# Kernel optimization log

Measured on AMD Instinct MI355X. Metric: run time of the kernel, lower is better.

Reference implementation:

```python
import jax, jax.numpy as jnp
import numpy as np

N, D = 8192, 128


def setup_inputs() -> dict:
    key = jax.random.key(0)
    k1, k2 = jax.random.split(key)
    z1 = jax.random.normal(k1, (N, D), dtype=jnp.float32)
    z2 = jax.random.normal(k2, (N, D), dtype=jnp.float32)
    return {"z1": z1, "z2": z2}


def reference(z1, z2):
    # logits[i, j] = -||z1_i - z2_j||^2, computed via the cdist-as-GEMM identity
    # (same math as dz = z2[None,:,:] - z1[:,None,:]; -einsum('...d,...d->...', dz, dz))
    sq1 = jnp.sum(z1 * z1, axis=-1)  # [N]
    sq2 = jnp.sum(z2 * z2, axis=-1)  # [N]
    logits = 2.0 * (z1 @ z2.T) - sq1[:, None] - sq2[None, :]  # [N, N]
    # CrossEntropyLoss with labels = arange(N): mean over rows of -log_softmax diag
    logp = jax.nn.log_softmax(logits, axis=-1)
    return -jnp.mean(jnp.diagonal(logp))
```

## Files before the change

kernel.cpp:

```cpp
#include <hip/hip_runtime.h>
#include <hip/hip_bf16.h>

typedef unsigned int   u32;
typedef unsigned short u16;

#define NN   8192
#define DD   128
#define CCH  32
#define CHUNK (NN / CCH)
#define JT   64
#define NT   (CHUNK / JT)
#define NIB  (NN / 256)

#define LOG2E 1.4426950408889634f
#define LN2F  0.6931471805599453f
#define BIAS  32.0f

typedef __bf16 bf16x8 __attribute__((ext_vector_type(8)));
typedef float  f32x16 __attribute__((ext_vector_type(16)));
typedef float  f32x2  __attribute__((ext_vector_type(2)));

__device__ __forceinline__ u16 f2bf(float x) {
    u32 u = __float_as_uint(x);
    u += 0x7fffu + ((u >> 16) & 1u);
    return (u16)(u >> 16);
}

__global__ __launch_bounds__(256) void prep_kernel(
    const float* __restrict__ z1, const float* __restrict__ z2,
    u32* __restrict__ b1, u32* __restrict__ b2,
    float* __restrict__ negsq2b, float* __restrict__ diag, u32* __restrict__ ctrl)
{
    if (blockIdx.x == 0 && threadIdx.x == 0) ctrl[0] = 0;
    int row  = blockIdx.x * 4 + (threadIdx.x >> 6);
    int lane = threadIdx.x & 63;
    float2 a = reinterpret_cast<const float2*>(z1)[row * 64 + lane];
    float2 b = reinterpret_cast<const float2*>(z2)[row * 64 + lane];
    b1[row * 64 + lane] = (u32)f2bf(a.x) | ((u32)f2bf(a.y) << 16);
    b2[row * 64 + lane] = (u32)f2bf(b.x) | ((u32)f2bf(b.y) << 16);
    float dot = a.x * b.x + a.y * b.y;
    float sq  = b.x * b.x + b.y * b.y;
    #pragma unroll
    for (int o = 32; o > 0; o >>= 1) {
        dot += __shfl_xor(dot, o);
        sq  += __shfl_xor(sq, o);
    }
    if (lane == 0) {
        negsq2b[row] = -sq * LOG2E - BIAS;
        diag[row]    = 2.0f * dot - sq;
    }
}

__global__ __launch_bounds__(256) void score_kernel(
    const u16* __restrict__ b1, const u16* __restrict__ b2,
    const float* __restrict__ negsq2b, float* __restrict__ partS)
{
    __shared__ alignas(16) u16 tile[3][JT * DD];
    __shared__ alignas(16) float nqs[CHUNK];
    const int tid  = threadIdx.x;
    const int lane = tid & 63;
    const int wid  = tid >> 6;
    const int r    = lane & 31, hi = lane >> 5;

    const int f     = blockIdx.x;
    const int chunk = (f >> 3) & 31;
    const int iblk  = (f & 7) * 4 + (f >> 8);
    const int j0    = chunk * CHUNK;
    const int i0w   = iblk * 256 + wid * 64;

    bf16x8 zf0[8], zf1[8];
    #pragma unroll
    for (int kk = 0; kk < 8; ++kk) {
        zf0[kk] = *reinterpret_cast<const bf16x8*>(b1 + (size_t)(i0w + r)      * DD + kk * 16 + hi * 8);
        zf1[kk] = *reinterpret_cast<const bf16x8*>(b1 + (size_t)(i0w + 32 + r) * DD + kk * 16 + hi * 8);
    }
    nqs[tid] = negsq2b[j0 + tid];
    __syncthreads();

    const int sl   = lane & 15;
    const int rrow = lane >> 4;

    auto stage = [&](int t, u16* dst_base) {
        #pragma unroll
        for (int u = 0; u < 4; ++u) {
            int row   = wid * 16 + u * 4 + rrow;
            int gslot = sl ^ (row & 15);
            const u16* src = b2 + (size_t)(j0 + t * JT + row) * DD + gslot * 8;
            __builtin_amdgcn_global_load_lds(
                (const __attribute__((address_space(1))) void*)src,
                (__attribute__((address_space(3))) void*)(dst_base + (wid * 16 + u * 4) * DD),
                16, 0, 0);
        }
    };

    stage(0, tile[0]);
    stage(1, tile[1]);

    float s0 = 0.f, s1 = 0.f, s2 = 0.f, s3 = 0.f;
    const f32x2 C2v = {2.0f * LOG2E, 2.0f * LOG2E};
    const int sw = r & 15;

    #pragma unroll
    for (int t = 0; t < NT; ++t) {
        if (t < NT - 1) asm volatile("s_waitcnt vmcnt(4)" ::: "memory");
        else            asm volatile("s_waitcnt vmcnt(0)" ::: "memory");
        __builtin_amdgcn_s_barrier();
        __builtin_amdgcn_sched_barrier(0);
        if (t + 2 < NT) stage(t + 2, tile[(t + 2) % 3]);
        const u16* tp = tile[t % 3];
        #pragma unroll
        for (int jj = 0; jj < 2; ++jj) {
            const float* nqb = &nqs[t * JT + jj * 32 + 4 * hi];
            float4 nq0 = *reinterpret_cast<const float4*>(nqb);
            float4 nq1 = *reinterpret_cast<const float4*>(nqb + 8);
            float4 nq2 = *reinterpret_cast<const float4*>(nqb + 16);
            float4 nq3 = *reinterpret_cast<const float4*>(nqb + 24);
            bf16x8 av[8];
            #pragma unroll
            for (int kk = 0; kk < 8; ++kk) {
                int off = (jj * 32 + r) * DD + (((2 * kk + hi) ^ sw) << 3);
                av[kk] = *reinterpret_cast<const bf16x8*>(tp + off);
            }
            f32x16 acc0 = {0.f}; f32x16 acc1 = {0.f};
            __builtin_amdgcn_s_setprio(1);
            #pragma unroll
            for (int kk = 0; kk < 8; ++kk) {
                acc0 = __builtin_amdgcn_mfma_f32_32x32x16_bf16(av[kk], zf0[kk], acc0, 0, 0, 0);
                acc1 = __builtin_amdgcn_mfma_f32_32x32x16_bf16(av[kk], zf1[kk], acc1, 0, 0, 0);
            }
            __builtin_amdgcn_s_setprio(0);
            const float nqa[16] = {nq0.x, nq0.y, nq0.z, nq0.w,
                                   nq1.x, nq1.y, nq1.z, nq1.w,
                                   nq2.x, nq2.y, nq2.z, nq2.w,
                                   nq3.x, nq3.y, nq3.z, nq3.w};
            #pragma unroll
            for (int q = 0; q < 8; ++q) {
                f32x2 n2 = {nqa[2 * q], nqa[2 * q + 1]};
                f32x2 a0 = {acc0[2 * q], acc0[2 * q + 1]};
                f32x2 t0 = a0 * C2v + n2;
                s0 += __builtin_amdgcn_exp2f(t0.x);
                s1 += __builtin_amdgcn_exp2f(t0.y);
                f32x2 a1 = {acc1[2 * q], acc1[2 * q + 1]};
                f32x2 t1 = a1 * C2v + n2;
                s2 += __builtin_amdgcn_exp2f(t1.x);
                s3 += __builtin_amdgcn_exp2f(t1.y);
            }
        }
    }

    float sum0 = s0 + s1, sum1 = s2 + s3;
    sum0 += __shfl_xor(sum0, 32);
    sum1 += __shfl_xor(sum1, 32);
    if (hi == 0) {
        partS[(size_t)chunk * NN + i0w + r]      = sum0;
        partS[(size_t)chunk * NN + i0w + 32 + r] = sum1;
    }
}

__global__ __launch_bounds__(256) void finalize1_kernel(
    const float* __restrict__ partS, const float* __restrict__ diag,
    float* __restrict__ blocksum, u32* __restrict__ ctrl, float* __restrict__ out)
{
    __shared__ float red[4];
    __shared__ u32 ticket;
    int r = blockIdx.x * 256 + threadIdx.x;
    float s = 0.f;
    #pragma unroll
    for (int c = 0; c < CCH; ++c) s += partS[(size_t)c * NN + r];
    float lse = (BIAS + __builtin_amdgcn_logf(s)) * LN2F;
    float acc = lse - diag[r];
    #pragma unroll
    for (int o = 32; o > 0; o >>= 1) acc += __shfl_xor(acc, o);
    int lane = threadIdx.x & 63, wid = threadIdx.x >> 6;
    if (lane == 0) red[wid] = acc;
    __syncthreads();
    if (threadIdx.x == 0) {
        blocksum[blockIdx.x] = red[0] + red[1] + red[2] + red[3];
        __threadfence();
        ticket = atomicAdd(ctrl, 1u);
    }
    __syncthreads();
    if (ticket == NIB - 1 && threadIdx.x == 0) {
        __threadfence();
        float v = 0.f;
        #pragma unroll
        for (int c = 0; c < NIB; ++c) v += blocksum[c];
        out[0] = v * (1.0f / (float)NN);
    }
}

extern "C" void kernel_launch(void* const* d_in, const int* in_sizes, int n_in,
                              void* d_out, int out_size, void* d_ws, size_t ws_size,
                              hipStream_t stream)
{
    const float* z1 = (const float*)d_in[0];
    const float* z2 = (const float*)d_in[1];
    char* ws = (char*)d_ws;

    const size_t bf_bytes = (size_t)NN * DD * 2;
    u32*   b1       = (u32*)ws;
    u32*   b2       = (u32*)(ws + bf_bytes);
    float* negsq2b  = (float*)(ws + 2 * bf_bytes);
    float* diag     = (float*)(ws + 2 * bf_bytes + (size_t)NN * 4);
    float* partS    = (float*)(ws + 2 * bf_bytes + (size_t)NN * 8);
    float* blocksum = (float*)(ws + 2 * bf_bytes + (size_t)NN * 8 + (size_t)CCH * NN * 4);
    u32*   ctrl     = (u32*)(ws + 2 * bf_bytes + (size_t)NN * 8 + (size_t)CCH * NN * 4 + 256);
    float* out      = (float*)d_out;

    prep_kernel<<<NN / 4, 256, 0, stream>>>(z1, z2, b1, b2, negsq2b, diag, ctrl);
    score_kernel<<<CCH * NIB, 256, 0, stream>>>((const u16*)b1, (const u16*)b2, negsq2b, partS);
    finalize1_kernel<<<NIB, 256, 0, stream>>>(partS, diag, blocksum, ctrl, out);
}
```

Baseline: 39.15 us.

## Switch score kernel to double-buffered LDS with occupancy hint and rolled loop

Replaces the triple-buffered LDS pipeline (explicit vmcnt waits and raw s_barrier) with a double buffer synchronised by __syncthreads. Adds a min-blocks-per-CU launch bound and removes the full unroll of the tile loop. Also interleaves LDS loads with the MFMAs and splits the exp accumulators into eight. The smaller LDS footprint and register cap are meant to allow more resident blocks, at the cost of only one tile of prefetch depth. The __syncthreads waits on all outstanding loads each iteration, so load latency is no longer overlapped as far ahead.

```diff
diff --git a/kernel.cpp b/kernel.cpp
--- a/kernel.cpp
+++ b/kernel.cpp
@@ -51,11 +51,11 @@
     }
 }
 
-__global__ __launch_bounds__(256) void score_kernel(
+__global__ __launch_bounds__(256, 3) void score_kernel(
     const u16* __restrict__ b1, const u16* __restrict__ b2,
     const float* __restrict__ negsq2b, float* __restrict__ partS)
 {
-    __shared__ alignas(16) u16 tile[3][JT * DD];
+    __shared__ alignas(16) u16 tile[2][JT * DD];
     __shared__ alignas(16) float nqs[CHUNK];
     const int tid  = threadIdx.x;
     const int lane = tid & 63;
@@ -75,12 +75,11 @@
         zf1[kk] = *reinterpret_cast<const bf16x8*>(b1 + (size_t)(i0w + 32 + r) * DD + kk * 16 + hi * 8);
     }
     nqs[tid] = negsq2b[j0 + tid];
-    __syncthreads();
 
     const int sl   = lane & 15;
     const int rrow = lane >> 4;
 
-    auto stage = [&](int t, u16* dst_base) {
+    auto stage = [&](int t, int buf) {
         #pragma unroll
         for (int u = 0; u < 4; ++u) {
             int row   = wid * 16 + u * 4 + rrow;
@@ -88,67 +87,60 @@
             const u16* src = b2 + (size_t)(j0 + t * JT + row) * DD + gslot * 8;
             __builtin_amdgcn_global_load_lds(
                 (const __attribute__((address_space(1))) void*)src,
-                (__attribute__((address_space(3))) void*)(dst_base + (wid * 16 + u * 4) * DD),
+                (__attribute__((address_space(3))) void*)(&tile[buf][(wid * 16 + u * 4) * DD]),
                 16, 0, 0);
         }
     };
 
-    stage(0, tile[0]);
-    stage(1, tile[1]);
-
     float s0 = 0.f, s1 = 0.f, s2 = 0.f, s3 = 0.f;
+    float q0 = 0.f, q1 = 0.f, q2 = 0.f, q3 = 0.f;
     const f32x2 C2v = {2.0f * LOG2E, 2.0f * LOG2E};
     const int sw = r & 15;
 
-    #pragma unroll
+    int cur = 0;
+    stage(0, 0);
     for (int t = 0; t < NT; ++t) {
-        if (t < NT - 1) asm volatile("s_waitcnt vmcnt(4)" ::: "memory");
-        else            asm volatile("s_waitcnt vmcnt(0)" ::: "memory");
-        __builtin_amdgcn_s_barrier();
-        __builtin_amdgcn_sched_barrier(0);
-        if (t + 2 < NT) stage(t + 2, tile[(t + 2) % 3]);
-        const u16* tp = tile[t % 3];
+        __syncthreads();
+        if (t + 1 < NT) stage(t + 1, cur ^ 1);
+        const u16* tp = tile[cur];
         #pragma unroll
         for (int jj = 0; jj < 2; ++jj) {
             const float* nqb = &nqs[t * JT + jj * 32 + 4 * hi];
-            float4 nq0 = *reinterpret_cast<const float4*>(nqb);
-            float4 nq1 = *reinterpret_cast<const float4*>(nqb + 8);
-            float4 nq2 = *reinterpret_cast<const float4*>(nqb + 16);
-            float4 nq3 = *reinterpret_cast<const float4*>(nqb + 24);
-            bf16x8 av[8];
+            const float4 nq0 = *reinterpret_cast<const float4*>(nqb);
+            const float4 nq1 = *reinterpret_cast<const float4*>(nqb + 8);
+            const float4 nq2 = *reinterpret_cast<const float4*>(nqb + 16);
+            const float4 nq3 = *reinterpret_cast<const float4*>(nqb + 24);
+            f32x16 acc0 = {0.f}; f32x16 acc1 = {0.f};
             #pragma unroll
             for (int kk = 0; kk < 8; ++kk) {
-                int off = (jj * 32 + r) * DD + (((2 * kk + hi) ^ sw) << 3);
-                av[kk] = *reinterpret_cast<const bf16x8*>(tp + off);
+                bf16x8 a = *reinterpret_cast<const bf16x8*>(
+                    tp + (jj * 32 + r) * DD + (((2 * kk + hi) ^ sw) << 3));
+                acc0 = __builtin_amdgcn_mfma_f32_32x32x16_bf16(a, zf0[kk], acc0, 0, 0, 0);
+                acc1 = __builtin_amdgcn_mfma_f32_32x32x16_bf16(a, zf1[kk], acc1, 0, 0, 0);
             }
-            f32x16 acc0 = {0.f}; f32x16 acc1 = {0.f};
-            __builtin_amdgcn_s_setprio(1);
             #pragma unroll
-            for (int kk = 0; kk < 8; ++kk) {
-                acc0 = __builtin_amdgcn_mfma_f32_32x32x16_bf16(av[kk], zf0[kk], acc0, 0, 0, 0);
-                acc1 = __builtin_amdgcn_mfma_f32_32x32x16_bf16(av[kk], zf1[kk], acc1, 0, 0, 0);
-            }
-            __builtin_amdgcn_s_setprio(0);
-            const float nqa[16] = {nq0.x, nq0.y, nq0.z, nq0.w,
-                                   nq1.x, nq1.y, nq1.z, nq1.w,
-                                   nq2.x, nq2.y, nq2.z, nq2.w,
-                                   nq3.x, nq3.y, nq3.z, nq3.w};
-            #pragma unroll
-            for (int q = 0; q < 8; ++q) {
-                f32x2 n2 = {nqa[2 * q], nqa[2 * q + 1]};
-                f32x2 a0 = {acc0[2 * q], acc0[2 * q + 1]};
-                f32x2 t0 = a0 * C2v + n2;
-                s0 += __builtin_amdgcn_exp2f(t0.x);
-                s1 += __builtin_amdgcn_exp2f(t0.y);
-                f32x2 a1 = {acc1[2 * q], acc1[2 * q + 1]};
-                f32x2 t1 = a1 * C2v + n2;
-                s2 += __builtin_amdgcn_exp2f(t1.x);
-                s3 += __builtin_amdgcn_exp2f(t1.y);
+            for (int m = 0; m < 4; ++m) {
+                const float4 nq = (m == 0) ? nq0 : (m == 1) ? nq1 : (m == 2) ? nq2 : nq3;
+                f32x2 n01 = {nq.x, nq.y}, n23 = {nq.z, nq.w};
+                f32x2 a01 = {acc0[4*m],   acc0[4*m+1]}, a23 = {acc0[4*m+2], acc0[4*m+3]};
+                f32x2 t01 = a01 * C2v + n01, t23 = a23 * C2v + n23;
+                s0 += __builtin_amdgcn_exp2f(t01.x);
+                s1 += __builtin_amdgcn_exp2f(t01.y);
+                s2 += __builtin_amdgcn_exp2f(t23.x);
+                s3 += __builtin_amdgcn_exp2f(t23.y);
+                f32x2 b01 = {acc1[4*m],   acc1[4*m+1]}, b23 = {acc1[4*m+2], acc1[4*m+3]};
+                f32x2 u01 = b01 * C2v + n01, u23 = b23 * C2v + n23;
+                q0 += __builtin_amdgcn_exp2f(u01.x);
+                q1 += __builtin_amdgcn_exp2f(u01.y);
+                q2 += __builtin_amdgcn_exp2f(u23.x);
+                q3 += __builtin_amdgcn_exp2f(u23.y);
             }
         }
-    }
-
-    float sum0 = s0 + s1, sum1 = s2 + s3;
+        cur ^= 1;
+    }
+
+    float sum0 = (s0 + s1) + (s2 + s3);
+    float sum1 = (q0 + q1) + (q2 + q3);
     sum0 += __shfl_xor(sum0, 32);
     sum1 += __shfl_xor(sum1, 32);
     if (hi == 0) {
```

Result: slower. 55.87 us (+42.7%).
